# Kernel tuning notes

Hardware: AMD Instinct MI355X
Metric: run time of the kernel (lower is better)

## Reference

```python
import jax, jax.numpy as jnp
import numpy as np

B, C, H, W = 32, 256, 64, 64
EPS = 1e-8  # clamp for cosine-similarity denominators


def setup_inputs() -> dict:
    key = jax.random.key(0)
    k1, k2, k3 = jax.random.split(key, 3)
    unmasked = jax.random.normal(k1, (B, C, H, W), dtype=jnp.float32)
    masked = jax.random.normal(k2, (B, C, H, W), dtype=jnp.float32)
    latent_mask = jax.random.randint(k3, (B, H, W), 0, 2, dtype=jnp.int32)
    return {
        "unmasked_latent_tensors": unmasked,
        "masked_latent_tensors": masked,
        "latent_mask": latent_mask,
    }


def reference(unmasked_latent_tensors, masked_latent_tensors, latent_mask):
    # Original torch code builds a full [B, B*H*W, H, W] cross-activation of a
    # cosine-similarity 1x1 conv (input vs. every masked position used as a
    # prototype), then gathers only the diagonal entries where batch index and
    # spatial position match. Mathematically that diagonal is just the
    # per-position cosine similarity along the channel axis, computed here
    # directly.
    u = unmasked_latent_tensors
    m = masked_latent_tensors
    num = jnp.sum(u * m, axis=1)                       # [B, H, W]
    u_norm = jnp.sqrt(jnp.sum(u * u, axis=1))          # [B, H, W]
    m_norm = jnp.sqrt(jnp.sum(m * m, axis=1))          # [B, H, W]
    sim = num / (jnp.maximum(u_norm, EPS) * jnp.maximum(m_norm, EPS))
    # masked=True: average similarity over mask==1 positions.
    mask_f = (latent_mask != 0).astype(sim.dtype)      # [B, H, W]
    return jnp.sum(sim * mask_f) / jnp.sum(mask_f)
```

## Files before the change

kernel.cpp:

```cpp
#include <hip/hip_runtime.h>


#define BB   32
#define CC   256
#define HH   64
#define WW   64
#define HWSZ (HH * WW)
#define NPOS (BB * HWSZ)
#define HW4  (HWSZ / 4)
#define PPB  256
#define NW   8
#define CPW  (CC / NW)
#define SIM_EPS 1e-8f

__global__ __launch_bounds__(512) void
sim_reduce_kernel(const float4* __restrict__ u4,
                  const float4* __restrict__ m4,
                  const int*    __restrict__ mask,
                  double*       __restrict__ ws)
{
    __shared__ float4 s_num[NW][64];
    __shared__ float4 s_uu [NW][64];
    __shared__ float4 s_mm [NW][64];

    const int wv = threadIdx.x >> 6;
    const int l  = threadIdx.x & 63;

    const int pos0 = blockIdx.x * PPB;
    const int b    = pos0 >> 12;
    const int hw0  = pos0 & (HWSZ - 1);

    const size_t base4 = (size_t)b * CC * HW4
                       + (size_t)(wv * CPW) * HW4
                       + (size_t)(hw0 >> 2) + (size_t)l;
    const float4* __restrict__ up = u4 + base4;
    const float4* __restrict__ mp = m4 + base4;

    float4 num = make_float4(0.f, 0.f, 0.f, 0.f);
    float4 uu  = make_float4(0.f, 0.f, 0.f, 0.f);
    float4 mm  = make_float4(0.f, 0.f, 0.f, 0.f);

#pragma unroll 4
    for (int c = 0; c < CPW; ++c) {
        const float4 a  = up[(size_t)c * HW4];
        const float4 bv = mp[(size_t)c * HW4];
        num.x = fmaf(a.x, bv.x, num.x);
        num.y = fmaf(a.y, bv.y, num.y);
        num.z = fmaf(a.z, bv.z, num.z);
        num.w = fmaf(a.w, bv.w, num.w);
        uu.x  = fmaf(a.x, a.x,  uu.x);
        uu.y  = fmaf(a.y, a.y,  uu.y);
        uu.z  = fmaf(a.z, a.z,  uu.z);
        uu.w  = fmaf(a.w, a.w,  uu.w);
        mm.x  = fmaf(bv.x, bv.x, mm.x);
        mm.y  = fmaf(bv.y, bv.y, mm.y);
        mm.z  = fmaf(bv.z, bv.z, mm.z);
        mm.w  = fmaf(bv.w, bv.w, mm.w);
    }

    s_num[wv][l] = num;
    s_uu [wv][l] = uu;
    s_mm [wv][l] = mm;
    __syncthreads();

    double sd = 0.0, md = 0.0;
    if (threadIdx.x < PPB) {
        const int t = threadIdx.x;
        float fn = 0.f, fu = 0.f, fm = 0.f;
#pragma unroll
        for (int k = 0; k < NW; ++k) {
            fn += ((const float*)s_num[k])[t];
            fu += ((const float*)s_uu [k])[t];
            fm += ((const float*)s_mm [k])[t];
        }
        const float denom = fmaxf(sqrtf(fu), SIM_EPS) * fmaxf(sqrtf(fm), SIM_EPS);
        const float sim   = fn / denom;
        if (mask[pos0 + t] != 0) { sd = (double)sim; md = 1.0; }
    }

#pragma unroll
    for (int off = 32; off > 0; off >>= 1) {
        sd += __shfl_down(sd, off, 64);
        md += __shfl_down(md, off, 64);
    }

    __shared__ double r_s[NW];
    __shared__ double r_m[NW];
    if (l == 0) { r_s[wv] = sd; r_m[wv] = md; }
    __syncthreads();

    if (threadIdx.x == 0) {
        double ts = 0.0, tm = 0.0;
#pragma unroll
        for (int k = 0; k < NW; ++k) { ts += r_s[k]; tm += r_m[k]; }
        atomicAdd(&ws[0], ts);
        atomicAdd(&ws[1], tm);
    }
}

__global__ void finalize_kernel(const double* __restrict__ ws,
                                float* __restrict__ out)
{
    out[0] = (float)(ws[0] / ws[1]);
}

extern "C" void kernel_launch(void* const* d_in, const int* in_sizes, int n_in,
                              void* d_out, int out_size, void* d_ws, size_t ws_size,
                              hipStream_t stream)
{
    const float4* u4   = (const float4*)d_in[0];
    const float4* m4   = (const float4*)d_in[1];
    const int*    mask = (const int*)d_in[2];
    float*  out = (float*)d_out;
    double* ws  = (double*)d_ws;

    hipMemsetAsync(d_ws, 0, 2 * sizeof(double), stream);

    sim_reduce_kernel<<<NPOS / PPB, 512, 0, stream>>>(u4, m4, mask, ws);
    finalize_kernel<<<1, 1, 0, stream>>>(ws, out);
}
```

Before: 281.8 us.

## Batch channel loads into register groups and fuse finalize via last-block counter

```diff
diff --git a/kernel.cpp b/kernel.cpp
--- a/kernel.cpp
+++ b/kernel.cpp
@@ -11,13 +11,17 @@
 #define PPB  256
 #define NW   8
 #define CPW  (CC / NW)
+#define NB   8
+#define NG   (CPW / NB)
+#define NBLK (NPOS / PPB)
 #define SIM_EPS 1e-8f
 
 __global__ __launch_bounds__(512) void
 sim_reduce_kernel(const float4* __restrict__ u4,
                   const float4* __restrict__ m4,
                   const int*    __restrict__ mask,
-                  double*       __restrict__ ws)
+                  double*       __restrict__ ws,
+                  float*        __restrict__ out)
 {
     __shared__ float4 s_num[NW][64];
     __shared__ float4 s_uu [NW][64];
@@ -40,22 +44,30 @@
     float4 uu  = make_float4(0.f, 0.f, 0.f, 0.f);
     float4 mm  = make_float4(0.f, 0.f, 0.f, 0.f);
 
-#pragma unroll 4
-    for (int c = 0; c < CPW; ++c) {
-        const float4 a  = up[(size_t)c * HW4];
-        const float4 bv = mp[(size_t)c * HW4];
-        num.x = fmaf(a.x, bv.x, num.x);
-        num.y = fmaf(a.y, bv.y, num.y);
-        num.z = fmaf(a.z, bv.z, num.z);
-        num.w = fmaf(a.w, bv.w, num.w);
-        uu.x  = fmaf(a.x, a.x,  uu.x);
-        uu.y  = fmaf(a.y, a.y,  uu.y);
-        uu.z  = fmaf(a.z, a.z,  uu.z);
-        uu.w  = fmaf(a.w, a.w,  uu.w);
-        mm.x  = fmaf(bv.x, bv.x, mm.x);
-        mm.y  = fmaf(bv.y, bv.y, mm.y);
-        mm.z  = fmaf(bv.z, bv.z, mm.z);
-        mm.w  = fmaf(bv.w, bv.w, mm.w);
+#pragma unroll
+    for (int g = 0; g < NG; ++g) {
+        float4 av[NB];
+        float4 bv[NB];
+#pragma unroll
+        for (int j = 0; j < NB; ++j) {
+            av[j] = up[(size_t)(g * NB + j) * HW4];
+            bv[j] = mp[(size_t)(g * NB + j) * HW4];
+        }
+#pragma unroll
+        for (int j = 0; j < NB; ++j) {
+            num.x = fmaf(av[j].x, bv[j].x, num.x);
+            num.y = fmaf(av[j].y, bv[j].y, num.y);
+            num.z = fmaf(av[j].z, bv[j].z, num.z);
+            num.w = fmaf(av[j].w, bv[j].w, num.w);
+            uu.x  = fmaf(av[j].x, av[j].x, uu.x);
+            uu.y  = fmaf(av[j].y, av[j].y, uu.y);
+            uu.z  = fmaf(av[j].z, av[j].z, uu.z);
+            uu.w  = fmaf(av[j].w, av[j].w, uu.w);
+            mm.x  = fmaf(bv[j].x, bv[j].x, mm.x);
+            mm.y  = fmaf(bv[j].y, bv[j].y, mm.y);
+            mm.z  = fmaf(bv[j].z, bv[j].z, mm.z);
+            mm.w  = fmaf(bv[j].w, bv[j].w, mm.w);
+        }
     }
 
     s_num[wv][l] = num;
@@ -95,13 +107,15 @@
         for (int k = 0; k < NW; ++k) { ts += r_s[k]; tm += r_m[k]; }
         atomicAdd(&ws[0], ts);
         atomicAdd(&ws[1], tm);
+        __threadfence();
+        const unsigned long long prev =
+            atomicAdd((unsigned long long*)&ws[2], 1ull);
+        if (prev == (unsigned long long)(NBLK - 1)) {
+            const double s  = atomicAdd(&ws[0], 0.0);
+            const double mc = atomicAdd(&ws[1], 0.0);
+            out[0] = (float)(s / mc);
+        }
     }
-}
-
-__global__ void finalize_kernel(const double* __restrict__ ws,
-                                float* __restrict__ out)
-{
-    out[0] = (float)(ws[0] / ws[1]);
 }
 
 extern "C" void kernel_launch(void* const* d_in, const int* in_sizes, int n_in,
@@ -114,8 +128,7 @@
     float*  out = (float*)d_out;
     double* ws  = (double*)d_ws;
 
-    hipMemsetAsync(d_ws, 0, 2 * sizeof(double), stream);
+    hipMemsetAsync(d_ws, 0, 3 * sizeof(double), stream);
 
-    sim_reduce_kernel<<<NPOS / PPB, 512, 0, stream>>>(u4, m4, mask, ws);
-    finalize_kernel<<<1, 1, 0, stream>>>(ws, out);
+    sim_reduce_kernel<<<NBLK, 512, 0, stream>>>(u4, m4, mask, ws, out);
 }
```

Result: slower. 299.6 us (+6.3%).
